# Kernel optimization log

Measured on AMD Instinct MI355X. Metric: run time of the kernel, lower is better.

Reference implementation:

```python
import jax, jax.numpy as jnp
from jax import lax
import numpy as np

NUM_HEADS = 8


def setup_inputs() -> dict:
    key = jax.random.key(0)
    k1, k2, k3, k4, k5 = jax.random.split(key, 5)
    L, B, E = 512, 32, 512
    return {
        "query": jax.random.normal(k1, (L, B, E), dtype=jnp.float32),
        "in_proj_weight": jax.random.normal(k2, (3 * E, E, 3), dtype=jnp.float32) * (1.0 / np.sqrt(3 * E)),
        "in_proj_bias": jax.random.normal(k3, (3 * E,), dtype=jnp.float32) * 0.02,
        "attention_weight": jax.random.uniform(k4, (B, L, L), dtype=jnp.float32),
        "bpps": jax.random.uniform(k5, (B, L, L), dtype=jnp.float32),
    }


def reference(query, in_proj_weight, in_proj_bias, attention_weight, bpps):
    # Faithful port of the custom multi_head_attention_forward self-attention path.
    # NOTE: attention_weight and bpps are accepted by the original signature but
    # never used in its body; dropout_p=0 / eval mode; no out_proj exists.
    tgt_len, bsz, embed_dim = query.shape
    num_heads = NUM_HEADS
    head_dim = embed_dim // num_heads
    scaling = float(head_dim) ** -0.5

    # conv1d QKV projection: input (bsz, embed, len), kernel (3*embed, embed, 3), padding 1
    x = jnp.transpose(query, (1, 2, 0))  # (B, E, L)
    qkv = lax.conv_general_dilated(
        x, in_proj_weight, window_strides=(1,), padding=[(1, 1)],
        dimension_numbers=("NCH", "OIH", "NCH"))
    qkv = qkv + in_proj_bias[None, :, None]  # (B, 3E, L)
    q, k, v = jnp.split(qkv, 3, axis=1)  # each (B, E, L)

    def to_heads(t):
        # (B, E, L) -> (L, B, E) -> (L, B*H, hd) -> (B*H, L, hd)
        t = jnp.transpose(t, (2, 0, 1))
        return jnp.transpose(t.reshape(tgt_len, bsz * num_heads, head_dim), (1, 0, 2))

    q = to_heads(q) * scaling
    k = to_heads(k)
    v = to_heads(v)

    scores = jnp.einsum("btd,bsd->bts", q, k)  # (B*H, L, L)
    attn = jax.nn.softmax(scores, axis=-1)
    out = jnp.einsum("bts,bsd->btd", attn, v)  # (B*H, L, hd)

    attn_output = jnp.transpose(out, (1, 0, 2)).reshape(tgt_len, bsz, embed_dim)
    avg_weights = attn.reshape(bsz, num_heads, tgt_len, tgt_len).sum(axis=1) / num_heads
    return attn_output, avg_weights
```

## Files before the change

### kernel.cpp

```cpp
#include <hip/hip_runtime.h>
#include <hip/hip_bf16.h>

typedef __hip_bfloat16 bf16;
typedef __attribute__((ext_vector_type(8))) __bf16 bf16x8;
typedef __attribute__((ext_vector_type(4))) float f32x4;

__device__ __forceinline__ void gl16(const void* g, void* l) {
  __builtin_amdgcn_global_load_lds((__attribute__((address_space(1))) void*)g,
                                   (__attribute__((address_space(3))) void*)l, 16, 0, 0);
}
__device__ __forceinline__ bf16 f2b(float f) { return __float2bfloat16(f); }

__device__ __forceinline__ int swz(int row, int bytecol) {
  return bytecol ^ ((row & 7) << 4);
}

__global__ void __launch_bounds__(256) prep_x(const float* __restrict__ q, bf16* __restrict__ Xb) {
  int row = blockIdx.x;
  int b = row >> 9, l = row & 511;
  int t = threadIdx.x;
  float2 v = *(const float2*)(q + (size_t)l * 16384 + b * 512 + t * 2);
  __hip_bfloat162 o2; o2.x = f2b(v.x); o2.y = f2b(v.y);
  *(__hip_bfloat162*)(Xb + (size_t)row * 512 + t * 2) = o2;
}

__global__ void __launch_bounds__(256) prep_w(const float* __restrict__ w, bf16* __restrict__ Wb) {
  int idx = blockIdx.x * 256 + threadIdx.x;
  int t = idx / 786432;
  int r = idx - t * 786432;
  int o = r >> 9, i = r & 511;
  Wb[idx] = f2b(w[(size_t)o * 1536 + i * 3 + t]);
}

__global__ void __launch_bounds__(256) conv_qkv(
    const bf16* __restrict__ Wb, const bf16* __restrict__ Xb,
    const float* __restrict__ bias, const char* __restrict__ zp,
    bf16* __restrict__ Qb, bf16* __restrict__ Kb, bf16* __restrict__ Vt) {
  __shared__ __align__(16) bf16 As[128 * 64];
  __shared__ __align__(16) bf16 Bs[128 * 64];
  const int tid = threadIdx.x;
  const int l0 = blockIdx.x * 128;
  const int o0 = blockIdx.y * 128;
  const int b  = blockIdx.z;
  const int lane = tid & 63, wid = tid >> 6;
  const int wm = (wid >> 1) * 64, wn = (wid & 1) * 64;
  const int lg = lane >> 4, lr = lane & 15;
  const int rsw = (lr & 7) << 4;

  f32x4 acc[4][4] = {};

  for (int step = 0; step < 24; ++step) {
    const int tap = step >> 3;
    const int k0 = (step & 7) * 64;
    #pragma unroll
    for (int it = 0; it < 4; ++it) {
      int ofs = tid * 16 + it * 4096;
      int row = ofs >> 7, bc = swz(row, ofs & 127);
      const char* src = (const char*)(Wb + (size_t)tap * 786432 + (size_t)(o0 + row) * 512 + k0) + bc;
      gl16(src, (char*)As + ofs);
    }
    #pragma unroll
    for (int it = 0; it < 4; ++it) {
      int ofs = tid * 16 + it * 4096;
      int row = ofs >> 7, bc = swz(row, ofs & 127);
      int l = l0 + row + tap - 1;
      const char* src = (l < 0 || l >= 512) ? (zp + bc)
                      : (const char*)(Xb + (size_t)(b * 512 + l) * 512 + k0) + bc;
      gl16(src, (char*)Bs + ofs);
    }
    __syncthreads();
    #pragma unroll
    for (int kk = 0; kk < 2; ++kk) {
      const int rcol = (kk * 64 + lg * 16) ^ rsw;
      bf16x8 a[4], bb[4];
      #pragma unroll
      for (int i = 0; i < 4; ++i)
        a[i] = *(const bf16x8*)((const char*)As + (wm + i * 16 + lr) * 128 + rcol);
      #pragma unroll
      for (int j = 0; j < 4; ++j)
        bb[j] = *(const bf16x8*)((const char*)Bs + (wn + j * 16 + lr) * 128 + rcol);
      #pragma unroll
      for (int i = 0; i < 4; ++i)
        #pragma unroll
        for (int j = 0; j < 4; ++j)
          acc[i][j] = __builtin_amdgcn_mfma_f32_16x16x32_bf16(a[i], bb[j], acc[i][j], 0, 0, 0);
    }
    __syncthreads();
  }

  const int part = o0 >> 9;
  #pragma unroll
  for (int i = 0; i < 4; ++i) {
    #pragma unroll
    for (int j = 0; j < 4; ++j) {
      int mbase = o0 + wm + i * 16 + lg * 4;
      int l = l0 + wn + j * 16 + lr;
      #pragma unroll
      for (int r = 0; r < 4; ++r) {
        int o = mbase + r;
        float v = acc[i][j][r] + bias[o];
        int rem = o & 511;
        int h = rem >> 6, d = rem & 63;
        size_t bh = (size_t)(b * 8 + h);
        if (part == 0)      Qb[(bh * 512 + l) * 64 + d] = f2b(v * 0.125f);
        else if (part == 1) Kb[(bh * 512 + l) * 64 + d] = f2b(v);
        else                Vt[(bh * 64 + d) * 512 + l] = f2b(v);
      }
    }
  }
}

__global__ void __launch_bounds__(256) flash_fwd(
    const bf16* __restrict__ Qb, const bf16* __restrict__ Kb, const bf16* __restrict__ Vt,
    float* __restrict__ out0, float* __restrict__ m_arr, float* __restrict__ li_arr) {
  __shared__ __align__(16) bf16 Qs[64 * 64];
  __shared__ __align__(16) bf16 Ks[64 * 64];
  __shared__ __align__(16) bf16 Vs[64 * 64];
  __shared__ __align__(16) bf16 Ps[4][16 * 72];
  const int tid = threadIdx.x;
  const int t0 = blockIdx.x * 64;
  const int bh = blockIdx.y;
  const int b = bh >> 3, h = bh & 7;
  const int lane = tid & 63, w = tid >> 6;
  const int lg = lane >> 4, lr = lane & 15;
  const int rsw = (lr & 7) << 4;

  #pragma unroll
  for (int it = 0; it < 2; ++it) {
    int ofs = tid * 16 + it * 4096;
    int row = ofs >> 7, bc = swz(row, ofs & 127);
    gl16((const char*)(Qb + ((size_t)bh * 512 + t0 + row) * 64) + bc, (char*)Qs + ofs);
  }

  float mreg[4] = {-1e30f, -1e30f, -1e30f, -1e30f};
  float lreg[4] = {0.f, 0.f, 0.f, 0.f};
  f32x4 oacc[4] = {};

  for (int sc = 0; sc < 8; ++sc) {
    __syncthreads();
    #pragma unroll
    for (int it = 0; it < 2; ++it) {
      int ofs = tid * 16 + it * 4096;
      int row = ofs >> 7, bc = swz(row, ofs & 127);
      gl16((const char*)(Kb + ((size_t)bh * 512 + sc * 64 + row) * 64) + bc, (char*)Ks + ofs);
      gl16((const char*)(Vt + ((size_t)bh * 64 + row) * 512 + sc * 64) + bc, (char*)Vs + ofs);
    }
    __syncthreads();

    bf16x8 aq[2];
    #pragma unroll
    for (int kk = 0; kk < 2; ++kk)
      aq[kk] = *(const bf16x8*)((const char*)Qs + (w * 16 + lr) * 128 + ((kk * 64 + lg * 16) ^ rsw));

    f32x4 s4[4] = {};
    #pragma unroll
    for (int j = 0; j < 4; ++j)
      #pragma unroll
      for (int kk = 0; kk < 2; ++kk) {
        bf16x8 bk = *(const bf16x8*)((const char*)Ks + (j * 16 + lr) * 128 + ((kk * 64 + lg * 16) ^ rsw));
        s4[j] = __builtin_amdgcn_mfma_f32_16x16x32_bf16(aq[kk], bk, s4[j], 0, 0, 0);
      }

    float cm[4], mnew[4], alpha[4], rs[4];
    #pragma unroll
    for (int r = 0; r < 4; ++r) {
      cm[r] = fmaxf(fmaxf(s4[0][r], s4[1][r]), fmaxf(s4[2][r], s4[3][r]));
      cm[r] = fmaxf(cm[r], __shfl_xor(cm[r], 1, 64));
      cm[r] = fmaxf(cm[r], __shfl_xor(cm[r], 2, 64));
      cm[r] = fmaxf(cm[r], __shfl_xor(cm[r], 4, 64));
      cm[r] = fmaxf(cm[r], __shfl_xor(cm[r], 8, 64));
      mnew[r] = fmaxf(mreg[r], cm[r]);
      alpha[r] = __expf(mreg[r] - mnew[r]);
      rs[r] = 0.f;
    }
    #pragma unroll
    for (int j = 0; j < 4; ++j)
      #pragma unroll
      for (int r = 0; r < 4; ++r) {
        float p = __expf(s4[j][r] - mnew[r]);
        s4[j][r] = p;
        rs[r] += p;
      }
    #pragma unroll
    for (int r = 0; r < 4; ++r) {
      rs[r] += __shfl_xor(rs[r], 1, 64);
      rs[r] += __shfl_xor(rs[r], 2, 64);
      rs[r] += __shfl_xor(rs[r], 4, 64);
      rs[r] += __shfl_xor(rs[r], 8, 64);
      lreg[r] = lreg[r] * alpha[r] + rs[r];
      mreg[r] = mnew[r];
    }
    #pragma unroll
    for (int j = 0; j < 4; ++j)
      #pragma unroll
      for (int r = 0; r < 4; ++r)
        oacc[j][r] *= alpha[r];

    #pragma unroll
    for (int j = 0; j < 4; ++j)
      #pragma unroll
      for (int r = 0; r < 4; ++r)
        Ps[w][(lg * 4 + r) * 72 + j * 16 + lr] = f2b(s4[j][r]);
    asm volatile("s_waitcnt lgkmcnt(0)" ::: "memory");
    __builtin_amdgcn_sched_barrier(0);

    bf16x8 pa[2];
    #pragma unroll
    for (int kk = 0; kk < 2; ++kk)
      pa[kk] = *(const bf16x8*)((const char*)&Ps[w][0] + lr * 144 + kk * 64 + lg * 16);

    #pragma unroll
    for (int j = 0; j < 4; ++j)
      #pragma unroll
      for (int kk = 0; kk < 2; ++kk) {
        bf16x8 bv = *(const bf16x8*)((const char*)Vs + (j * 16 + lr) * 128 + ((kk * 64 + lg * 16) ^ rsw));
        oacc[j] = __builtin_amdgcn_mfma_f32_16x16x32_bf16(pa[kk], bv, oacc[j], 0, 0, 0);
      }
  }

  float il[4];
  #pragma unroll
  for (int r = 0; r < 4; ++r) il[r] = 1.f / lreg[r];

  #pragma unroll
  for (int j = 0; j < 4; ++j)
    #pragma unroll
    for (int r = 0; r < 4; ++r) {
      int t = t0 + w * 16 + lg * 4 + r;
      out0[(size_t)t * 16384 + (size_t)b * 512 + h * 64 + j * 16 + lr] = oacc[j][r] * il[r];
    }
  if (lr == 0) {
    #pragma unroll
    for (int r = 0; r < 4; ++r) {
      int t = t0 + w * 16 + lg * 4 + r;
      m_arr[bh * 512 + t] = mreg[r];
      li_arr[bh * 512 + t] = il[r];
    }
  }
}

__global__ void __launch_bounds__(256) avg_attn(
    const bf16* __restrict__ Qb, const bf16* __restrict__ Kb,
    const float* __restrict__ m_arr, const float* __restrict__ li_arr,
    float* __restrict__ out1) {
  __shared__ __align__(16) bf16 Qs[64 * 64];
  __shared__ __align__(16) bf16 Ks[128 * 64];
  const int tid = threadIdx.x;
  const int s0 = blockIdx.x * 128;
  const int t0 = blockIdx.y * 64;
  const int b  = blockIdx.z;
  const int lane = tid & 63, w = tid >> 6;
  const int lg = lane >> 4, lr = lane & 15;
  const int rsw = (lr & 7) << 4;

  f32x4 avg4[8] = {};

  for (int h = 0; h < 8; ++h) {
    int bh = b * 8 + h;
    __syncthreads();
    #pragma unroll
    for (int it = 0; it < 2; ++it) {
      int ofs = tid * 16 + it * 4096;
      int row = ofs >> 7, bc = swz(row, ofs & 127);
      gl16((const char*)(Qb + ((size_t)bh * 512 + t0 + row) * 64) + bc, (char*)Qs + ofs);
    }
    #pragma unroll
    for (int it = 0; it < 4; ++it) {
      int ofs = tid * 16 + it * 4096;
      int row = ofs >> 7, bc = swz(row, ofs & 127);
      gl16((const char*)(Kb + ((size_t)bh * 512 + s0 + row) * 64) + bc, (char*)Ks + ofs);
    }
    __syncthreads();

    float mv[4], iv[4];
    #pragma unroll
    for (int r = 0; r < 4; ++r) {
      int t = t0 + w * 16 + lg * 4 + r;
      mv[r] = m_arr[bh * 512 + t];
      iv[r] = li_arr[bh * 512 + t];
    }

    bf16x8 aq[2];
    #pragma unroll
    for (int kk = 0; kk < 2; ++kk)
      aq[kk] = *(const bf16x8*)((const char*)Qs + (w * 16 + lr) * 128 + ((kk * 64 + lg * 16) ^ rsw));

    #pragma unroll
    for (int j = 0; j < 8; ++j) {
      f32x4 s4 = {};
      #pragma unroll
      for (int kk = 0; kk < 2; ++kk) {
        bf16x8 bk = *(const bf16x8*)((const char*)Ks + (j * 16 + lr) * 128 + ((kk * 64 + lg * 16) ^ rsw));
        s4 = __builtin_amdgcn_mfma_f32_16x16x32_bf16(aq[kk], bk, s4, 0, 0, 0);
      }
      #pragma unroll
      for (int r = 0; r < 4; ++r)
        avg4[j][r] += __expf(s4[r] - mv[r]) * iv[r];
    }
  }

  #pragma unroll
  for (int j = 0; j < 8; ++j)
    #pragma unroll
    for (int r = 0; r < 4; ++r) {
      int t = t0 + w * 16 + lg * 4 + r;
      out1[((size_t)b * 512 + t) * 512 + s0 + j * 16 + lr] = avg4[j][r] * 0.125f;
    }
}

extern "C" void kernel_launch(void* const* d_in, const int* in_sizes, int n_in,
                              void* d_out, int out_size, void* d_ws, size_t ws_size,
                              hipStream_t stream) {
  const float* query = (const float*)d_in[0];
  const float* wconv = (const float*)d_in[1];
  const float* bias  = (const float*)d_in[2];

  char* ws = (char*)d_ws;
  bf16* Xb  = (bf16*)(ws + 0);
  bf16* Wb  = (bf16*)(ws + 16777216);
  bf16* Qb  = (bf16*)(ws + 21495808);
  bf16* Kb  = (bf16*)(ws + 38273024);
  bf16* Vt  = (bf16*)(ws + 55050240);
  float* m_arr  = (float*)(ws + 71827456);
  float* li_arr = (float*)(ws + 72351744);
  char* zp = ws + 72876032;

  float* out0 = (float*)d_out;
  float* out1 = out0 + 8388608;

  hipMemsetAsync(zp, 0, 4096, stream);
  prep_x<<<16384, 256, 0, stream>>>(query, Xb);
  prep_w<<<9216, 256, 0, stream>>>(wconv, Wb);
  conv_qkv<<<dim3(4, 12, 32), 256, 0, stream>>>(Wb, Xb, bias, zp, Qb, Kb, Vt);
  flash_fwd<<<dim3(8, 256), 256, 0, stream>>>(Qb, Kb, Vt, out0, m_arr, li_arr);
  avg_attn<<<dim3(4, 8, 32), 256, 0, stream>>>(Qb, Kb, m_arr, li_arr, out1);
}
```

Baseline: 355.6 us.

## Load conv QKV MFMA fragments directly from global memory, bypassing LDS

The conv_qkv GEMM no longer stages weight and input tiles through swizzled shared memory with global_load_lds and block barriers. Each lane now reads its bf16x8 MFMA fragments straight from global memory, using per-tap row pointers and a zero-pad pointer for out-of-range sequence positions. The goal is to remove the LDS round trip and the __syncthreads stalls. In exchange, waves sharing a tile load the same data twice, the loads are less coalesced and depend on L1/L2 hits, and the zero-pad buffer must now cover a full 512-element row.

```diff
diff --git a/kernel.cpp b/kernel.cpp
--- a/kernel.cpp
+++ b/kernel.cpp
@@ -36,8 +36,6 @@
     const bf16* __restrict__ Wb, const bf16* __restrict__ Xb,
     const float* __restrict__ bias, const char* __restrict__ zp,
     bf16* __restrict__ Qb, bf16* __restrict__ Kb, bf16* __restrict__ Vt) {
-  __shared__ __align__(16) bf16 As[128 * 64];
-  __shared__ __align__(16) bf16 Bs[128 * 64];
   const int tid = threadIdx.x;
   const int l0 = blockIdx.x * 128;
   const int o0 = blockIdx.y * 128;
@@ -45,47 +43,40 @@
   const int lane = tid & 63, wid = tid >> 6;
   const int wm = (wid >> 1) * 64, wn = (wid & 1) * 64;
   const int lg = lane >> 4, lr = lane & 15;
-  const int rsw = (lr & 7) << 4;
 
   f32x4 acc[4][4] = {};
 
-  for (int step = 0; step < 24; ++step) {
-    const int tap = step >> 3;
-    const int k0 = (step & 7) * 64;
-    #pragma unroll
-    for (int it = 0; it < 4; ++it) {
-      int ofs = tid * 16 + it * 4096;
-      int row = ofs >> 7, bc = swz(row, ofs & 127);
-      const char* src = (const char*)(Wb + (size_t)tap * 786432 + (size_t)(o0 + row) * 512 + k0) + bc;
-      gl16(src, (char*)As + ofs);
-    }
-    #pragma unroll
-    for (int it = 0; it < 4; ++it) {
-      int ofs = tid * 16 + it * 4096;
-      int row = ofs >> 7, bc = swz(row, ofs & 127);
-      int l = l0 + row + tap - 1;
-      const char* src = (l < 0 || l >= 512) ? (zp + bc)
-                      : (const char*)(Xb + (size_t)(b * 512 + l) * 512 + k0) + bc;
-      gl16(src, (char*)Bs + ofs);
-    }
-    __syncthreads();
-    #pragma unroll
-    for (int kk = 0; kk < 2; ++kk) {
-      const int rcol = (kk * 64 + lg * 16) ^ rsw;
-      bf16x8 a[4], bb[4];
-      #pragma unroll
-      for (int i = 0; i < 4; ++i)
-        a[i] = *(const bf16x8*)((const char*)As + (wm + i * 16 + lr) * 128 + rcol);
-      #pragma unroll
-      for (int j = 0; j < 4; ++j)
-        bb[j] = *(const bf16x8*)((const char*)Bs + (wn + j * 16 + lr) * 128 + rcol);
-      #pragma unroll
-      for (int i = 0; i < 4; ++i)
+  for (int tap = 0; tap < 3; ++tap) {
+    const bf16* ab[4];
+    const bf16* bbp[4];
+    #pragma unroll
+    for (int i = 0; i < 4; ++i)
+      ab[i] = Wb + (size_t)tap * 786432 + (size_t)(o0 + wm + i * 16 + lr) * 512 + lg * 8;
+    #pragma unroll
+    for (int j = 0; j < 4; ++j) {
+      int l = l0 + wn + j * 16 + lr + tap - 1;
+      const bf16* p = (l < 0 || l >= 512) ? (const bf16*)zp
+                                          : Xb + (size_t)(b * 512 + l) * 512;
+      bbp[j] = p + lg * 8;
+    }
+    #pragma unroll
+    for (int k0 = 0; k0 < 512; k0 += 64) {
+      #pragma unroll
+      for (int kk = 0; kk < 2; ++kk) {
+        bf16x8 a[4], bv[4];
+        #pragma unroll
+        for (int i = 0; i < 4; ++i)
+          a[i] = *(const bf16x8*)(ab[i] + k0 + kk * 32);
         #pragma unroll
         for (int j = 0; j < 4; ++j)
-          acc[i][j] = __builtin_amdgcn_mfma_f32_16x16x32_bf16(a[i], bb[j], acc[i][j], 0, 0, 0);
-    }
-    __syncthreads();
+          bv[j] = *(const bf16x8*)(bbp[j] + k0 + kk * 32);
+        #pragma unroll
+        for (int i = 0; i < 4; ++i)
+          #pragma unroll
+          for (int j = 0; j < 4; ++j)
+            acc[i][j] = __builtin_amdgcn_mfma_f32_16x16x32_bf16(a[i], bv[j], acc[i][j], 0, 0, 0);
+      }
+    }
   }
 
   const int part = o0 >> 9;
```

After: 519.2 us. +46.0%, slower.

## Double-buffer conv QKV tiles and use zero-padded input to drop boundary checks

Applied to the files above, without the earlier changes.

Adds two LDS buffers to the conv projection GEMM so the next K-step's tiles are loaded while MFMAs run on the current one, and removes one barrier per step. It also writes the bf16 input into a per-batch layout padded by one row on each side, which removes the per-row bounds check and the separate zero page. In exchange, the whole padded buffer (about 16.8MB) is now memset each call and LDS use doubles, which may lower occupancy.

```diff
diff --git a/kernel.cpp b/kernel.cpp
--- a/kernel.cpp
+++ b/kernel.cpp
@@ -15,13 +15,13 @@
   return bytecol ^ ((row & 7) << 4);
 }
 
-__global__ void __launch_bounds__(256) prep_x(const float* __restrict__ q, bf16* __restrict__ Xb) {
+__global__ void __launch_bounds__(256) prep_x(const float* __restrict__ q, bf16* __restrict__ Xp) {
   int row = blockIdx.x;
   int b = row >> 9, l = row & 511;
   int t = threadIdx.x;
   float2 v = *(const float2*)(q + (size_t)l * 16384 + b * 512 + t * 2);
   __hip_bfloat162 o2; o2.x = f2b(v.x); o2.y = f2b(v.y);
-  *(__hip_bfloat162*)(Xb + (size_t)row * 512 + t * 2) = o2;
+  *(__hip_bfloat162*)(Xp + ((size_t)(b * 514 + l + 1)) * 512 + t * 2) = o2;
 }
 
 __global__ void __launch_bounds__(256) prep_w(const float* __restrict__ w, bf16* __restrict__ Wb) {
@@ -33,11 +33,11 @@
 }
 
 __global__ void __launch_bounds__(256) conv_qkv(
-    const bf16* __restrict__ Wb, const bf16* __restrict__ Xb,
-    const float* __restrict__ bias, const char* __restrict__ zp,
+    const bf16* __restrict__ Wb, const bf16* __restrict__ Xp,
+    const float* __restrict__ bias,
     bf16* __restrict__ Qb, bf16* __restrict__ Kb, bf16* __restrict__ Vt) {
-  __shared__ __align__(16) bf16 As[128 * 64];
-  __shared__ __align__(16) bf16 Bs[128 * 64];
+  __shared__ __align__(16) bf16 As[2][128 * 64];
+  __shared__ __align__(16) bf16 Bs[2][128 * 64];
   const int tid = threadIdx.x;
   const int l0 = blockIdx.x * 128;
   const int o0 = blockIdx.y * 128;
@@ -49,43 +49,47 @@
 
   f32x4 acc[4][4] = {};
 
-  for (int step = 0; step < 24; ++step) {
+  auto STAGE = [&](int step, int buf) {
     const int tap = step >> 3;
     const int k0 = (step & 7) * 64;
+    const char* wbase = (const char*)Wb + ((size_t)tap * 786432 + (size_t)o0 * 512 + k0) * 2;
+    const char* xbase = (const char*)Xp + (((size_t)(b * 514 + l0 + tap)) * 512 + k0) * 2;
     #pragma unroll
     for (int it = 0; it < 4; ++it) {
       int ofs = tid * 16 + it * 4096;
       int row = ofs >> 7, bc = swz(row, ofs & 127);
-      const char* src = (const char*)(Wb + (size_t)tap * 786432 + (size_t)(o0 + row) * 512 + k0) + bc;
-      gl16(src, (char*)As + ofs);
+      gl16(wbase + (size_t)row * 1024 + bc, (char*)&As[buf][0] + ofs);
     }
     #pragma unroll
     for (int it = 0; it < 4; ++it) {
       int ofs = tid * 16 + it * 4096;
       int row = ofs >> 7, bc = swz(row, ofs & 127);
-      int l = l0 + row + tap - 1;
-      const char* src = (l < 0 || l >= 512) ? (zp + bc)
-                      : (const char*)(Xb + (size_t)(b * 512 + l) * 512 + k0) + bc;
-      gl16(src, (char*)Bs + ofs);
-    }
-    __syncthreads();
+      gl16(xbase + (size_t)row * 1024 + bc, (char*)&Bs[buf][0] + ofs);
+    }
+  };
+
+  STAGE(0, 0);
+  int cur = 0;
+  for (int step = 0; step < 24; ++step) {
+    __syncthreads();
+    if (step < 23) STAGE(step + 1, cur ^ 1);
     #pragma unroll
     for (int kk = 0; kk < 2; ++kk) {
       const int rcol = (kk * 64 + lg * 16) ^ rsw;
       bf16x8 a[4], bb[4];
       #pragma unroll
       for (int i = 0; i < 4; ++i)
-        a[i] = *(const bf16x8*)((const char*)As + (wm + i * 16 + lr) * 128 + rcol);
+        a[i] = *(const bf16x8*)((const char*)&As[cur][0] + (wm + i * 16 + lr) * 128 + rcol);
       #pragma unroll
       for (int j = 0; j < 4; ++j)
-        bb[j] = *(const bf16x8*)((const char*)Bs + (wn + j * 16 + lr) * 128 + rcol);
+        bb[j] = *(const bf16x8*)((const char*)&Bs[cur][0] + (wn + j * 16 + lr) * 128 + rcol);
       #pragma unroll
       for (int i = 0; i < 4; ++i)
         #pragma unroll
         for (int j = 0; j < 4; ++j)
           acc[i][j] = __builtin_amdgcn_mfma_f32_16x16x32_bf16(a[i], bb[j], acc[i][j], 0, 0, 0);
     }
-    __syncthreads();
+    cur ^= 1;
   }
 
   const int part = o0 >> 9;
@@ -316,22 +320,21 @@
   const float* bias  = (const float*)d_in[2];
 
   char* ws = (char*)d_ws;
-  bf16* Xb  = (bf16*)(ws + 0);
-  bf16* Wb  = (bf16*)(ws + 16777216);
-  bf16* Qb  = (bf16*)(ws + 21495808);
-  bf16* Kb  = (bf16*)(ws + 38273024);
-  bf16* Vt  = (bf16*)(ws + 55050240);
-  float* m_arr  = (float*)(ws + 71827456);
-  float* li_arr = (float*)(ws + 72351744);
-  char* zp = ws + 72876032;
+  bf16* Xp  = (bf16*)(ws + 0);
+  bf16* Wb  = (bf16*)(ws + 16842752);
+  bf16* Qb  = (bf16*)(ws + 21561344);
+  bf16* Kb  = (bf16*)(ws + 38338560);
+  bf16* Vt  = (bf16*)(ws + 55115776);
+  float* m_arr  = (float*)(ws + 71892992);
+  float* li_arr = (float*)(ws + 72417280);
 
   float* out0 = (float*)d_out;
   float* out1 = out0 + 8388608;
 
-  hipMemsetAsync(zp, 0, 4096, stream);
-  prep_x<<<16384, 256, 0, stream>>>(query, Xb);
+  hipMemsetAsync(Xp, 0, 16842752, stream);
+  prep_x<<<16384, 256, 0, stream>>>(query, Xp);
   prep_w<<<9216, 256, 0, stream>>>(wconv, Wb);
-  conv_qkv<<<dim3(4, 12, 32), 256, 0, stream>>>(Wb, Xb, bias, zp, Qb, Kb, Vt);
+  conv_qkv<<<dim3(4, 12, 32), 256, 0, stream>>>(Wb, Xp, bias, Qb, Kb, Vt);
   flash_fwd<<<dim3(8, 256), 256, 0, stream>>>(Qb, Kb, Vt, out0, m_arr, li_arr);
   avg_attn<<<dim3(4, 8, 32), 256, 0, stream>>>(Qb, Kb, m_arr, li_arr, out1);
 }
```

New measurement: 363.4 us. 1.02x slower.
